# Kernel tuning notes

Measured on AMD Instinct MI355X. Metric: run time of the kernel, lower is better.

## Reference

```python
import jax, jax.numpy as jnp
import numpy as np

B, N, E, C1, C2 = 8, 4096, 2048, 128, 128
DENSITY = 0.05  # incidence matrix sparsity (stored dense, as in the original)


def setup_inputs() -> dict:
    key = jax.random.key(0)
    kx, kh, kw = jax.random.split(key, 3)
    x = jax.random.normal(kx, (B, N, C1), dtype=jnp.float32)
    # binary hypergraph incidence matrix [B, n_node, n_edge]
    H = (jax.random.uniform(kh, (B, N, E)) < DENSITY).astype(jnp.float32)
    W = jax.random.normal(kw, (C1, C2), dtype=jnp.float32) * 0.02
    b = jnp.zeros((C2,), dtype=jnp.float32)
    return {"x": x, "H": H, "W": W, "b": b}


def _mean_agg(path, X):
    # path: [B, T, S], X: [B, S, D] -> mean-aggregated [B, T, D]
    out = jnp.matmul(path, X)
    s = jnp.sum(path, axis=2, keepdims=True)  # [B, T, 1]
    # 1/s with inf (s==0) masked to 0, fused as a single where
    return jnp.where(s > 0, out / s, jnp.zeros_like(out))


def reference(x, H, W, b):
    # fc: [B, N, C1] -> [B, N, C2]
    x = jnp.matmul(x, W) + b
    # v2e: aggregate node features into hyperedge features
    Ht = jnp.swapaxes(H, 1, 2)  # [B, E, N]
    e = _mean_agg(Ht, x)        # [B, E, C2]
    # e2v: aggregate hyperedge features back to nodes
    v = _mean_agg(H, e)         # [B, N, C2]
    return v
```

## Files before the change

### kernel.cpp

```cpp
#include <hip/hip_runtime.h>
#include <stdint.h>

constexpr int B_ = 8, N_ = 4096, E_ = 2048, C_ = 128;
constexpr int KT  = 32;
constexpr int MT  = 64;
constexpr int NJW = 4;
constexpr int LRP = 65;

typedef short bf16x8 __attribute__((ext_vector_type(8)));
typedef float f32x4  __attribute__((ext_vector_type(4)));
typedef unsigned int u32x4 __attribute__((ext_vector_type(4)));

__device__ inline uint16_t bf16_rne(float f) {
    uint32_t u = __builtin_bit_cast(uint32_t, f);
    return (uint16_t)((u + 0x7FFFu + ((u >> 16) & 1u)) >> 16);
}

constexpr size_t BIT_B = (size_t)(N_ / 32) * E_;
constexpr size_t HT_E  = (size_t)B_ * BIT_B;
constexpr size_t WT_E  = (size_t)C_ * C_;
constexpr size_t EBF_E = (size_t)B_ * C_ * E_;
constexpr size_t RS_E  = (size_t)B_ * E_;
constexpr size_t RD_E  = (size_t)B_ * N_;

__global__ void pack_kernel(const float* __restrict__ H, uint32_t* __restrict__ HT,
                            uint32_t* __restrict__ HTe) {
    const int t  = threadIdx.x;
    const int eg = blockIdx.x & 7;
    const int ng = (blockIdx.x >> 3) & 127;
    const int b  = blockIdx.x >> 10;
    const int e  = eg * 256 + t;
    const float* hp = H + ((size_t)b * N_ + ng * 32) * E_ + e;
    uint32_t w = 0;
#pragma unroll
    for (int i = 0; i < 32; ++i) w |= (hp[(size_t)i * E_] > 0.5f) ? (1u << i) : 0u;
    HT[((size_t)b * (N_ / 32) + ng) * E_ + e] = w;

    const int lane  = t & 63;
    const int ebase = eg * 256 + (t >> 6) * 64;
    uint32_t val = 0;
#pragma unroll
    for (int i = 0; i < 32; ++i) {
        unsigned long long m = __ballot((w >> i) & 1u);
        uint32_t half = (lane < 32) ? (uint32_t)m : (uint32_t)(m >> 32);
        if ((lane & 31) == i) val = half;
    }
    HTe[((size_t)b * (E_ / 32) + (ebase >> 5) + (lane >> 5)) * N_ + ng * 32 + (lane & 31)] = val;
}

__global__ void prep_kernel(const float* __restrict__ W, const uint32_t* __restrict__ HT,
                            const uint32_t* __restrict__ HTe, uint16_t* __restrict__ WTb,
                            float* __restrict__ rs_e, float* __restrict__ rd_n) {
    const int blk = blockIdx.x, t = threadIdx.x;
    if (blk < 128) {
        const int i = blk * 256 + t;
        const int b = i >> 12, n = i & 4095;
        const uint32_t* p = HTe + (size_t)b * BIT_B + n;
        int s = 0;
#pragma unroll 1
        for (int ew = 0; ew < E_ / 32; ++ew) s += __popc(p[(size_t)ew * N_]);
        rd_n[i] = (s > 0) ? 0.5f / (float)s : 0.f;
    } else if (blk < 192) {
        const int i = (blk - 128) * 256 + t;
        const int b = i >> 11, e = i & 2047;
        const uint32_t* p = HT + (size_t)b * BIT_B + e;
        int s = 0;
#pragma unroll 1
        for (int ng = 0; ng < N_ / 32; ++ng) s += __popc(p[(size_t)ng * E_]);
        rs_e[i] = (s > 0) ? 0.5f / (float)s : 0.f;
    } else if (blk < 256) {
        const int i = (blk - 192) * 256 + t;
        const int c = i >> 7, k = i & 127;
        WTb[i] = bf16_rne(W[k * C_ + c]);
    }
}


#define LOADA(S, k0_) do {                                                            \
    if constexpr (MODE == 0) {                                                        \
        _Pragma("unroll")                                                             \
        for (int g = 0; g < NG; ++g) {                                                \
            const float* ap = Ax + ((size_t)batch * N_ + m0 + g * 16 + l15) * C_ + (k0_) + quad * 8; \
            const float4 f0 = *(const float4*)ap;                                     \
            const float4 f1 = *(const float4*)(ap + 4);                               \
            af##S[g*8+0]=f0.x; af##S[g*8+1]=f0.y; af##S[g*8+2]=f0.z; af##S[g*8+3]=f0.w; \
            af##S[g*8+4]=f1.x; af##S[g*8+5]=f1.y; af##S[g*8+6]=f1.z; af##S[g*8+7]=f1.w; \
        }                                                                             \
    } else {                                                                          \
        const uint32_t* p = Hp + (size_t)((k0_) >> 5) * RL + m0 + l15;                \
        _Pragma("unroll")                                                             \
        for (int g = 0; g < NG; ++g) aw##S[g] = p[g * 16];                            \
    } } while (0)

#define LOADB(S, k0_) do {                                                            \
    _Pragma("unroll")                                                                 \
    for (int j2 = 0; j2 < NJW; ++j2)                                                  \
        bq##S[j2] = *(const bf16x8*)&Bp[(size_t)((jw + j2) * 16 + l15) * K + (k0_) + quad * 8]; \
    } while (0)

#define MKFRAGS(S, A)                                                                 \
    bf16x8 A[NG];                                                                     \
    do {                                                                              \
    if constexpr (MODE == 0) {                                                        \
        _Pragma("unroll")                                                             \
        for (int g = 0; g < NG; ++g)                                                  \
            { _Pragma("unroll")                                                       \
              for (int jj = 0; jj < 8; ++jj) A[g][jj] = (short)bf16_rne(af##S[g*8+jj]); } \
    } else {                                                                          \
        const int qs = quad * 8;                                                      \
        _Pragma("unroll")                                                             \
        for (int g = 0; g < NG; ++g) {                                                \
            const uint32_t wv = aw##S[g];                                             \
            const uint32_t nb0 = (wv >> qs) & 0xFu;                                   \
            const uint32_t nb1 = (wv >> (qs + 4)) & 0xFu;                             \
            const uint32_t s0m = ((nb0 * 0x204081u) & 0x01010101u) << 6;              \
            const uint32_t s1m = ((nb1 * 0x204081u) & 0x01010101u) << 6;              \
            u32x4 qq = { __builtin_amdgcn_perm(s0m, 0u, 0x05000400u),                 \
                         __builtin_amdgcn_perm(s0m, 0u, 0x07000600u),                 \
                         __builtin_amdgcn_perm(s1m, 0u, 0x05000400u),                 \
                         __builtin_amdgcn_perm(s1m, 0u, 0x07000600u) };               \
            A[g] = __builtin_bit_cast(bf16x8, qq);                                    \
        }                                                                             \
    } } while (0)

template <int MODE>
__device__ __attribute__((always_inline))
void gemm_body(const float* __restrict__ Ax, const uint32_t* __restrict__ bits,
               const uint16_t* __restrict__ Btb, const float* __restrict__ bias,
               const float* __restrict__ rcp, uint16_t* __restrict__ outT,
               float* __restrict__ outF) {
    constexpr int K   = (MODE == 0) ? C_ : (MODE == 1) ? N_ : E_;
    constexpr int KH  = K / 2;
    constexpr int SW  = KH / KT;
    constexpr int OLD = (MODE == 0) ? N_ : E_;
    constexpr int RL  = (MODE == 1) ? E_ : N_;
    constexpr int NG  = MT / 16;
    static_assert(SW == 2 || (SW >= 4 && SW % 4 == 0), "pipeline shape");

    __shared__ float R[2 * 64 * LRP];

    const int t = threadIdx.x, wave = t >> 6, lane = t & 63;
    const int l15 = lane & 15, quad = lane >> 4;
    const int kh = wave & 1, jg = wave >> 1;
    const int jw = jg * NJW;
    const int kwv = kh * KH;
    const int batch = blockIdx.x & 7;
    const int m0 = (blockIdx.x >> 3) * MT;

    const uint16_t* Bp = Btb + (MODE == 0 ? (size_t)0 : (size_t)batch * C_ * K);
    const uint32_t* Hp = bits + (size_t)batch * BIT_B;

    f32x4 acc[NG * NJW];
    float    af0[NG * 8], af1[NG * 8], af2[NG * 8], af3[NG * 8];
    uint32_t aw0[NG], aw1[NG], aw2[NG], aw3[NG];
    bf16x8   bq0[NJW], bq1[NJW], bq2[NJW], bq3[NJW];

    auto mfma_all = [&](const bf16x8 (&A)[NG], const bf16x8 (&bv)[NJW])
        __attribute__((always_inline)) {
#pragma unroll
        for (int j2 = 0; j2 < NJW; ++j2)
#pragma unroll
            for (int g = 0; g < NG; ++g)
                acc[g * NJW + j2] = __builtin_amdgcn_mfma_f32_16x16x32_bf16(A[g], bv[j2], acc[g * NJW + j2], 0, 0, 0);
    };

#pragma unroll
    for (int i = 0; i < NG * NJW; ++i) acc[i] = (f32x4){0.f, 0.f, 0.f, 0.f};

    if constexpr (SW >= 4) {
        LOADA(0, kwv);          LOADB(0, kwv);
        LOADA(1, kwv + KT);     LOADB(1, kwv + KT);
        LOADA(2, kwv + 2 * KT); LOADB(2, kwv + 2 * KT);
        LOADA(3, kwv + 3 * KT); LOADB(3, kwv + 3 * KT);
#pragma unroll 1
        for (int s = 0; s < SW - 4; s += 4) {
            { MKFRAGS(0, A0); mfma_all(A0, bq0); LOADA(0, kwv + (s + 4) * KT); LOADB(0, kwv + (s + 4) * KT); }
            { MKFRAGS(1, A1); mfma_all(A1, bq1); LOADA(1, kwv + (s + 5) * KT); LOADB(1, kwv + (s + 5) * KT); }
            { MKFRAGS(2, A2); mfma_all(A2, bq2); LOADA(2, kwv + (s + 6) * KT); LOADB(2, kwv + (s + 6) * KT); }
            { MKFRAGS(3, A3); mfma_all(A3, bq3); LOADA(3, kwv + (s + 7) * KT); LOADB(3, kwv + (s + 7) * KT); }
        }
        { MKFRAGS(0, A0); mfma_all(A0, bq0); }
        { MKFRAGS(1, A1); mfma_all(A1, bq1); }
        { MKFRAGS(2, A2); mfma_all(A2, bq2); }
        { MKFRAGS(3, A3); mfma_all(A3, bq3); }
    } else {
        LOADA(0, kwv);      LOADB(0, kwv);
        LOADA(1, kwv + KT); LOADB(1, kwv + KT);
        { MKFRAGS(0, A0); mfma_all(A0, bq0); }
        { MKFRAGS(1, A1); mfma_all(A1, bq1); }
    }

    const int rbase = jg * 64 * LRP;
    if (kh == 1) {
#pragma unroll
        for (int g = 0; g < NG; ++g)
#pragma unroll
            for (int j2 = 0; j2 < NJW; ++j2)
#pragma unroll
                for (int r = 0; r < 4; ++r)
                    R[rbase + (g * 16 + quad * 4 + r) * LRP + j2 * 16 + l15] = acc[g * NJW + j2][r];
    }
    __syncthreads();
    if (kh != 0) return;
#pragma unroll
    for (int g = 0; g < NG; ++g)
#pragma unroll
        for (int j2 = 0; j2 < NJW; ++j2)
#pragma unroll
            for (int r = 0; r < 4; ++r)
                acc[g * NJW + j2][r] += R[rbase + (g * 16 + quad * 4 + r) * LRP + j2 * 16 + l15];

    float mul[NG][4];
    if constexpr (MODE != 0) {
#pragma unroll
        for (int g = 0; g < NG; ++g) {
            const float4 rv = *(const float4*)&rcp[(size_t)batch * RL + m0 + g * 16 + quad * 4];
            mul[g][0] = rv.x; mul[g][1] = rv.y; mul[g][2] = rv.z; mul[g][3] = rv.w;
        }
    }
#pragma unroll
    for (int g = 0; g < NG; ++g) {
        const int row = m0 + g * 16 + quad * 4;
        if constexpr (MODE == 2) {
            float* op = outF + ((size_t)batch * N_ + row) * C_;
#pragma unroll
            for (int j2 = 0; j2 < NJW; ++j2) {
                const int c = (jw + j2) * 16 + l15;
#pragma unroll
                for (int r = 0; r < 4; ++r) op[(size_t)r * C_ + c] = acc[g * NJW + j2][r] * mul[g][r];
            }
        } else {
#pragma unroll
            for (int j2 = 0; j2 < NJW; ++j2) {
                const int c = (jw + j2) * 16 + l15;
                float v0, v1, v2, v3;
                if constexpr (MODE == 0) {
                    float bb = bias[c];
                    v0 = acc[g * NJW + j2][0] + bb; v1 = acc[g * NJW + j2][1] + bb;
                    v2 = acc[g * NJW + j2][2] + bb; v3 = acc[g * NJW + j2][3] + bb;
                } else {
                    v0 = acc[g * NJW + j2][0] * mul[g][0]; v1 = acc[g * NJW + j2][1] * mul[g][1];
                    v2 = acc[g * NJW + j2][2] * mul[g][2]; v3 = acc[g * NJW + j2][3] * mul[g][3];
                }
                uint32_t q0 = (uint32_t)bf16_rne(v0) | ((uint32_t)bf16_rne(v1) << 16);
                uint32_t q1 = (uint32_t)bf16_rne(v2) | ((uint32_t)bf16_rne(v3) << 16);
                uint16_t* op = outT + ((size_t)batch * C_ + c) * OLD + row;
                *(uint2*)op = make_uint2(q0, q1);
            }
        }
    }
}

__global__ __launch_bounds__(256, 2)
void fc_k(const float* __restrict__ Ax, const uint16_t* __restrict__ Btb,
          const float* __restrict__ bias, uint16_t* __restrict__ outT) {
    gemm_body<0>(Ax, nullptr, Btb, bias, nullptr, outT, nullptr);
}
__global__ __launch_bounds__(256, 2)
void v2e_k(const uint32_t* __restrict__ HT, const uint16_t* __restrict__ Btb,
           const float* __restrict__ rcp, uint16_t* __restrict__ outT) {
    gemm_body<1>(nullptr, HT, Btb, nullptr, rcp, outT, nullptr);
}
__global__ __launch_bounds__(256, 2)
void e2v_k(const uint32_t* __restrict__ HTe, const uint16_t* __restrict__ Btb,
           const float* __restrict__ rcp, float* __restrict__ outF) {
    gemm_body<2>(nullptr, HTe, Btb, nullptr, rcp, nullptr, outF);
}

extern "C" void kernel_launch(void* const* d_in, const int* in_sizes, int n_in,
                              void* d_out, int out_size, void* d_ws, size_t ws_size,
                              hipStream_t stream) {
    const float* x    = (const float*)d_in[0];
    const float* H    = (const float*)d_in[1];
    const float* W    = (const float*)d_in[2];
    const float* bias = (const float*)d_in[3];
    float* out = (float*)d_out;

    uint32_t* HT   = (uint32_t*)d_ws;
    uint32_t* HTe  = HT + HT_E;
    uint16_t* WTb  = (uint16_t*)(HTe + HT_E);
    uint16_t* ebfT = WTb + WT_E;
    float*    rs_e = (float*)(ebfT + EBF_E);
    float*    rd_n = rs_e + RS_E;
    uint16_t* xwbT = (uint16_t*)d_out;

    pack_kernel<<<dim3(8192), dim3(256), 0, stream>>>(H, HT, HTe);
    prep_kernel<<<dim3(256), dim3(256), 0, stream>>>(W, HT, HTe, WTb, rs_e, rd_n);
    fc_k <<<dim3(8 * (N_ / MT)), dim3(256), 0, stream>>>(x, WTb, bias, xwbT);
    v2e_k<<<dim3(8 * (E_ / MT)), dim3(256), 0, stream>>>(HT, xwbT, rs_e, ebfT);
    e2v_k<<<dim3(8 * (N_ / MT)), dim3(256), 0, stream>>>(HTe, ebfT, rd_n, out);
}
```

Before: 465.7 us.

## Fuse H packing with fc GEMM and move bit transpose into prep kernel

The fc GEMM now runs as extra blocks inside the H-packing launch and converts W to bf16 on the fly, which removes the separate fc launch and the WTb buffer. Packing now reads float4 and writes uint4, so each thread handles four edges. The ballot-based bit transpose (HTe) and the per-node degree counts move into the prep kernel, which builds them from HT instead of rereading H. Fewer launches and wider loads on the dominant 268MB read of H are the intent. The cost is strided scalar W reads inside the fc blocks and a larger prep kernel that rereads HT.

New measurement: 477.5 us. 2.5% more time.

```diff
diff --git a/kernel.cpp b/kernel.cpp
--- a/kernel.cpp
+++ b/kernel.cpp
@@ -4,8 +4,8 @@
 constexpr int B_ = 8, N_ = 4096, E_ = 2048, C_ = 128;
 constexpr int KT  = 32;
 constexpr int MT  = 64;
-constexpr int NJW = 4;
 constexpr int LRP = 65;
+constexpr int PACK_BLKS = 2048;
 
 typedef short bf16x8 __attribute__((ext_vector_type(8)));
 typedef float f32x4  __attribute__((ext_vector_type(4)));
@@ -18,62 +18,9 @@
 
 constexpr size_t BIT_B = (size_t)(N_ / 32) * E_;
 constexpr size_t HT_E  = (size_t)B_ * BIT_B;
-constexpr size_t WT_E  = (size_t)C_ * C_;
 constexpr size_t EBF_E = (size_t)B_ * C_ * E_;
 constexpr size_t RS_E  = (size_t)B_ * E_;
 constexpr size_t RD_E  = (size_t)B_ * N_;
-
-__global__ void pack_kernel(const float* __restrict__ H, uint32_t* __restrict__ HT,
-                            uint32_t* __restrict__ HTe) {
-    const int t  = threadIdx.x;
-    const int eg = blockIdx.x & 7;
-    const int ng = (blockIdx.x >> 3) & 127;
-    const int b  = blockIdx.x >> 10;
-    const int e  = eg * 256 + t;
-    const float* hp = H + ((size_t)b * N_ + ng * 32) * E_ + e;
-    uint32_t w = 0;
-#pragma unroll
-    for (int i = 0; i < 32; ++i) w |= (hp[(size_t)i * E_] > 0.5f) ? (1u << i) : 0u;
-    HT[((size_t)b * (N_ / 32) + ng) * E_ + e] = w;
-
-    const int lane  = t & 63;
-    const int ebase = eg * 256 + (t >> 6) * 64;
-    uint32_t val = 0;
-#pragma unroll
-    for (int i = 0; i < 32; ++i) {
-        unsigned long long m = __ballot((w >> i) & 1u);
-        uint32_t half = (lane < 32) ? (uint32_t)m : (uint32_t)(m >> 32);
-        if ((lane & 31) == i) val = half;
-    }
-    HTe[((size_t)b * (E_ / 32) + (ebase >> 5) + (lane >> 5)) * N_ + ng * 32 + (lane & 31)] = val;
-}
-
-__global__ void prep_kernel(const float* __restrict__ W, const uint32_t* __restrict__ HT,
-                            const uint32_t* __restrict__ HTe, uint16_t* __restrict__ WTb,
-                            float* __restrict__ rs_e, float* __restrict__ rd_n) {
-    const int blk = blockIdx.x, t = threadIdx.x;
-    if (blk < 128) {
-        const int i = blk * 256 + t;
-        const int b = i >> 12, n = i & 4095;
-        const uint32_t* p = HTe + (size_t)b * BIT_B + n;
-        int s = 0;
-#pragma unroll 1
-        for (int ew = 0; ew < E_ / 32; ++ew) s += __popc(p[(size_t)ew * N_]);
-        rd_n[i] = (s > 0) ? 0.5f / (float)s : 0.f;
-    } else if (blk < 192) {
-        const int i = (blk - 128) * 256 + t;
-        const int b = i >> 11, e = i & 2047;
-        const uint32_t* p = HT + (size_t)b * BIT_B + e;
-        int s = 0;
-#pragma unroll 1
-        for (int ng = 0; ng < N_ / 32; ++ng) s += __popc(p[(size_t)ng * E_]);
-        rs_e[i] = (s > 0) ? 0.5f / (float)s : 0.f;
-    } else if (blk < 256) {
-        const int i = (blk - 192) * 256 + t;
-        const int c = i >> 7, k = i & 127;
-        WTb[i] = bf16_rne(W[k * C_ + c]);
-    }
-}
 
 
 #define LOADA(S, k0_) do {                                                            \
@@ -93,10 +40,19 @@
     } } while (0)
 
 #define LOADB(S, k0_) do {                                                            \
-    _Pragma("unroll")                                                                 \
-    for (int j2 = 0; j2 < NJW; ++j2)                                                  \
-        bq##S[j2] = *(const bf16x8*)&Bp[(size_t)((jw + j2) * 16 + l15) * K + (k0_) + quad * 8]; \
-    } while (0)
+    if constexpr (MODE == 0) {                                                        \
+        _Pragma("unroll")                                                             \
+        for (int j2 = 0; j2 < NJWm; ++j2) {                                           \
+            const int c = (jw + j2) * 16 + l15;                                       \
+            _Pragma("unroll")                                                         \
+            for (int jj = 0; jj < 8; ++jj)                                            \
+                bq##S[j2][jj] = (short)bf16_rne(Wf[(size_t)((k0_) + quad * 8 + jj) * C_ + c]); \
+        }                                                                             \
+    } else {                                                                          \
+        _Pragma("unroll")                                                             \
+        for (int j2 = 0; j2 < NJWm; ++j2)                                             \
+            bq##S[j2] = *(const bf16x8*)&Bp[(size_t)((jw + j2) * 16 + l15) * K + (k0_) + quad * 8]; \
+    } } while (0)
 
 #define MKFRAGS(S, A)                                                                 \
     bf16x8 A[NG];                                                                     \
@@ -125,49 +81,57 @@
 
 template <int MODE>
 __device__ __attribute__((always_inline))
-void gemm_body(const float* __restrict__ Ax, const uint32_t* __restrict__ bits,
-               const uint16_t* __restrict__ Btb, const float* __restrict__ bias,
-               const float* __restrict__ rcp, uint16_t* __restrict__ outT,
-               float* __restrict__ outF) {
-    constexpr int K   = (MODE == 0) ? C_ : (MODE == 1) ? N_ : E_;
-    constexpr int KH  = K / 2;
-    constexpr int SW  = KH / KT;
-    constexpr int OLD = (MODE == 0) ? N_ : E_;
-    constexpr int RL  = (MODE == 1) ? E_ : N_;
-    constexpr int NG  = MT / 16;
-    static_assert(SW == 2 || (SW >= 4 && SW % 4 == 0), "pipeline shape");
-
-    __shared__ float R[2 * 64 * LRP];
+void gemm_body(int bid, const float* __restrict__ Ax, const uint32_t* __restrict__ bits,
+               const uint16_t* __restrict__ Btb, const float* __restrict__ Wf,
+               const float* __restrict__ bias, const float* __restrict__ rcp,
+               uint16_t* __restrict__ outT, float* __restrict__ outF) {
+    constexpr int K    = (MODE == 0) ? C_ : (MODE == 1) ? N_ : E_;
+    constexpr int NJWm = (MODE == 0) ? 2 : 4;
+    constexpr int KH   = (MODE == 0) ? K : K / 2;
+    constexpr int SW   = KH / KT;
+    constexpr int OLD  = (MODE == 0) ? N_ : E_;
+    constexpr int RL   = (MODE == 1) ? E_ : N_;
+    constexpr int NG   = MT / 16;
+
+    __shared__ float R[(MODE == 0) ? 1 : (2 * 64 * LRP)];
 
     const int t = threadIdx.x, wave = t >> 6, lane = t & 63;
     const int l15 = lane & 15, quad = lane >> 4;
-    const int kh = wave & 1, jg = wave >> 1;
-    const int jw = jg * NJW;
+    const int kh = (MODE == 0) ? 0 : (wave & 1);
+    const int jg = (MODE == 0) ? wave : (wave >> 1);
+    const int jw = jg * NJWm;
     const int kwv = kh * KH;
-    const int batch = blockIdx.x & 7;
-    const int m0 = (blockIdx.x >> 3) * MT;
+    const int batch = bid & 7;
+    const int m0 = (bid >> 3) * MT;
 
     const uint16_t* Bp = Btb + (MODE == 0 ? (size_t)0 : (size_t)batch * C_ * K);
     const uint32_t* Hp = bits + (size_t)batch * BIT_B;
 
-    f32x4 acc[NG * NJW];
+    f32x4 acc[NG * NJWm];
     float    af0[NG * 8], af1[NG * 8], af2[NG * 8], af3[NG * 8];
     uint32_t aw0[NG], aw1[NG], aw2[NG], aw3[NG];
-    bf16x8   bq0[NJW], bq1[NJW], bq2[NJW], bq3[NJW];
-
-    auto mfma_all = [&](const bf16x8 (&A)[NG], const bf16x8 (&bv)[NJW])
+    bf16x8   bq0[NJWm], bq1[NJWm], bq2[NJWm], bq3[NJWm];
+
+    auto mfma_all = [&](const bf16x8 (&A)[NG], const bf16x8 (&bv)[NJWm])
         __attribute__((always_inline)) {
 #pragma unroll
-        for (int j2 = 0; j2 < NJW; ++j2)
+        for (int j2 = 0; j2 < NJWm; ++j2)
 #pragma unroll
             for (int g = 0; g < NG; ++g)
-                acc[g * NJW + j2] = __builtin_amdgcn_mfma_f32_16x16x32_bf16(A[g], bv[j2], acc[g * NJW + j2], 0, 0, 0);
+                acc[g * NJWm + j2] = __builtin_amdgcn_mfma_f32_16x16x32_bf16(A[g], bv[j2], acc[g * NJWm + j2], 0, 0, 0);
     };
 
 #pragma unroll
-    for (int i = 0; i < NG * NJW; ++i) acc[i] = (f32x4){0.f, 0.f, 0.f, 0.f};
-
-    if constexpr (SW >= 4) {
+    for (int i = 0; i < NG * NJWm; ++i) acc[i] = (f32x4){0.f, 0.f, 0.f, 0.f};
+
+    if constexpr (MODE == 0) {
+        LOADA(0, 0);  LOADB(0, 0);
+        LOADA(1, KT); LOADB(1, KT);
+        { MKFRAGS(0, A0); mfma_all(A0, bq0); LOADA(0, 2 * KT); LOADB(0, 2 * KT); }
+        { MKFRAGS(1, A1); mfma_all(A1, bq1); LOADA(1, 3 * KT); LOADB(1, 3 * KT); }
+        { MKFRAGS(0, A0); mfma_all(A0, bq0); }
+        { MKFRAGS(1, A1); mfma_all(A1, bq1); }
+    } else {
         LOADA(0, kwv);          LOADB(0, kwv);
         LOADA(1, kwv + KT);     LOADB(1, kwv + KT);
         LOADA(2, kwv + 2 * KT); LOADB(2, kwv + 2 * KT);
@@ -183,32 +147,27 @@
         { MKFRAGS(1, A1); mfma_all(A1, bq1); }
         { MKFRAGS(2, A2); mfma_all(A2, bq2); }
         { MKFRAGS(3, A3); mfma_all(A3, bq3); }
-    } else {
-        LOADA(0, kwv);      LOADB(0, kwv);
-        LOADA(1, kwv + KT); LOADB(1, kwv + KT);
-        { MKFRAGS(0, A0); mfma_all(A0, bq0); }
-        { MKFRAGS(1, A1); mfma_all(A1, bq1); }
-    }
-
-    const int rbase = jg * 64 * LRP;
-    if (kh == 1) {
+
+        const int rbase = jg * 64 * LRP;
+        if (kh == 1) {
+#pragma unroll
+            for (int g = 0; g < NG; ++g)
+#pragma unroll
+                for (int j2 = 0; j2 < NJWm; ++j2)
+#pragma unroll
+                    for (int r = 0; r < 4; ++r)
+                        R[rbase + (g * 16 + quad * 4 + r) * LRP + j2 * 16 + l15] = acc[g * NJWm + j2][r];
+        }
+        __syncthreads();
+        if (kh != 0) return;
 #pragma unroll
         for (int g = 0; g < NG; ++g)
 #pragma unroll
-            for (int j2 = 0; j2 < NJW; ++j2)
+            for (int j2 = 0; j2 < NJWm; ++j2)
 #pragma unroll
                 for (int r = 0; r < 4; ++r)
-                    R[rbase + (g * 16 + quad * 4 + r) * LRP + j2 * 16 + l15] = acc[g * NJW + j2][r];
-    }
-    __syncthreads();
-    if (kh != 0) return;
-#pragma unroll
-    for (int g = 0; g < NG; ++g)
-#pragma unroll
-        for (int j2 = 0; j2 < NJW; ++j2)
-#pragma unroll
-            for (int r = 0; r < 4; ++r)
-                acc[g * NJW + j2][r] += R[rbase + (g * 16 + quad * 4 + r) * LRP + j2 * 16 + l15];
+                    acc[g * NJWm + j2][r] += R[rbase + (g * 16 + quad * 4 + r) * LRP + j2 * 16 + l15];
+    }
 
     float mul[NG][4];
     if constexpr (MODE != 0) {
@@ -224,23 +183,23 @@
         if constexpr (MODE == 2) {
             float* op = outF + ((size_t)batch * N_ + row) * C_;
 #pragma unroll
-            for (int j2 = 0; j2 < NJW; ++j2) {
+            for (int j2 = 0; j2 < NJWm; ++j2) {
                 const int c = (jw + j2) * 16 + l15;
 #pragma unroll
-                for (int r = 0; r < 4; ++r) op[(size_t)r * C_ + c] = acc[g * NJW + j2][r] * mul[g][r];
+                for (int r = 0; r < 4; ++r) op[(size_t)r * C_ + c] = acc[g * NJWm + j2][r] * mul[g][r];
             }
         } else {
 #pragma unroll
-            for (int j2 = 0; j2 < NJW; ++j2) {
+            for (int j2 = 0; j2 < NJWm; ++j2) {
                 const int c = (jw + j2) * 16 + l15;
                 float v0, v1, v2, v3;
                 if constexpr (MODE == 0) {
                     float bb = bias[c];
-                    v0 = acc[g * NJW + j2][0] + bb; v1 = acc[g * NJW + j2][1] + bb;
-                    v2 = acc[g * NJW + j2][2] + bb; v3 = acc[g * NJW + j2][3] + bb;
+                    v0 = acc[g * NJWm + j2][0] + bb; v1 = acc[g * NJWm + j2][1] + bb;
+                    v2 = acc[g * NJWm + j2][2] + bb; v3 = acc[g * NJWm + j2][3] + bb;
                 } else {
-                    v0 = acc[g * NJW + j2][0] * mul[g][0]; v1 = acc[g * NJW + j2][1] * mul[g][1];
-                    v2 = acc[g * NJW + j2][2] * mul[g][2]; v3 = acc[g * NJW + j2][3] * mul[g][3];
+                    v0 = acc[g * NJWm + j2][0] * mul[g][0]; v1 = acc[g * NJWm + j2][1] * mul[g][1];
+                    v2 = acc[g * NJWm + j2][2] * mul[g][2]; v3 = acc[g * NJWm + j2][3] * mul[g][3];
                 }
                 uint32_t q0 = (uint32_t)bf16_rne(v0) | ((uint32_t)bf16_rne(v1) << 16);
                 uint32_t q1 = (uint32_t)bf16_rne(v2) | ((uint32_t)bf16_rne(v3) << 16);
@@ -252,19 +211,84 @@
 }
 
 __global__ __launch_bounds__(256, 2)
-void fc_k(const float* __restrict__ Ax, const uint16_t* __restrict__ Btb,
-          const float* __restrict__ bias, uint16_t* __restrict__ outT) {
-    gemm_body<0>(Ax, nullptr, Btb, bias, nullptr, outT, nullptr);
-}
+void pack_fc_k(const float* __restrict__ H, uint32_t* __restrict__ HT,
+               const float* __restrict__ x, const float* __restrict__ W,
+               const float* __restrict__ bias, uint16_t* __restrict__ xwbT) {
+    if (blockIdx.x >= PACK_BLKS) {
+        gemm_body<0>(blockIdx.x - PACK_BLKS, x, nullptr, nullptr, W, bias, nullptr, xwbT, nullptr);
+        return;
+    }
+    const int t  = threadIdx.x;
+    const int eg = blockIdx.x & 1;
+    const int ng = (blockIdx.x >> 1) & 127;
+    const int b  = blockIdx.x >> 8;
+    const int e0 = eg * 1024 + t * 4;
+    const float* hp = H + ((size_t)b * N_ + ng * 32) * E_ + e0;
+    uint32_t w0 = 0, w1 = 0, w2 = 0, w3 = 0;
+#pragma unroll
+    for (int i = 0; i < 32; ++i) {
+        const float4 f = *(const float4*)(hp + (size_t)i * E_);
+        w0 |= (f.x > 0.5f) ? (1u << i) : 0u;
+        w1 |= (f.y > 0.5f) ? (1u << i) : 0u;
+        w2 |= (f.z > 0.5f) ? (1u << i) : 0u;
+        w3 |= (f.w > 0.5f) ? (1u << i) : 0u;
+    }
+    *(uint4*)&HT[((size_t)b * (N_ / 32) + ng) * E_ + e0] = make_uint4(w0, w1, w2, w3);
+}
+
+__global__ void prep_kernel(const uint32_t* __restrict__ HT, uint32_t* __restrict__ HTe,
+                            float* __restrict__ rs_e, float* __restrict__ rd_n) {
+    const int blk = blockIdx.x, t = threadIdx.x;
+    const int wave = t >> 6, lane = t & 63;
+    if (blk < 256) {
+        const int wid = blk * 4 + wave;
+        const int b = wid >> 7, ng = wid & 127;
+        const uint32_t* p = HT + ((size_t)b * (N_ / 32) + ng) * E_;
+        int cnt = 0;
+#pragma unroll 1
+        for (int c8 = 0; c8 < E_ / 64; ++c8) {
+            const uint32_t w = p[c8 * 64 + lane];
+#pragma unroll
+            for (int i = 0; i < 32; ++i) {
+                unsigned long long m = __ballot((w >> i) & 1u);
+                if (lane == i) cnt += __popcll(m);
+            }
+        }
+        if (lane < 32)
+            rd_n[(size_t)b * N_ + ng * 32 + lane] = (cnt > 0) ? 0.5f / (float)cnt : 0.f;
+    } else if (blk < 320) {
+        const int i = (blk - 256) * 256 + t;
+        const int b = i >> 11, e = i & 2047;
+        const uint32_t* p = HT + (size_t)b * BIT_B + e;
+        int s = 0;
+#pragma unroll 1
+        for (int ng = 0; ng < N_ / 32; ++ng) s += __popc(p[(size_t)ng * E_]);
+        rs_e[i] = (s > 0) ? 0.5f / (float)s : 0.f;
+    } else {
+        const int wid = (blk - 320) * 4 + wave;
+        const int b = wid >> 12, rest = wid & 4095;
+        const int ng = rest >> 5, eg64 = rest & 31;
+        const uint32_t w = HT[((size_t)b * (N_ / 32) + ng) * E_ + eg64 * 64 + lane];
+        uint32_t val = 0;
+#pragma unroll
+        for (int i = 0; i < 32; ++i) {
+            unsigned long long m = __ballot((w >> i) & 1u);
+            uint32_t half = (lane < 32) ? (uint32_t)m : (uint32_t)(m >> 32);
+            if ((lane & 31) == i) val = half;
+        }
+        HTe[((size_t)b * (E_ / 32) + eg64 * 2 + (lane >> 5)) * N_ + ng * 32 + (lane & 31)] = val;
+    }
+}
+
 __global__ __launch_bounds__(256, 2)
 void v2e_k(const uint32_t* __restrict__ HT, const uint16_t* __restrict__ Btb,
            const float* __restrict__ rcp, uint16_t* __restrict__ outT) {
-    gemm_body<1>(nullptr, HT, Btb, nullptr, rcp, outT, nullptr);
+    gemm_body<1>(blockIdx.x, nullptr, HT, Btb, nullptr, nullptr, rcp, outT, nullptr);
 }
 __global__ __launch_bounds__(256, 2)
 void e2v_k(const uint32_t* __restrict__ HTe, const uint16_t* __restrict__ Btb,
            const float* __restrict__ rcp, float* __restrict__ outF) {
-    gemm_body<2>(nullptr, HTe, Btb, nullptr, rcp, nullptr, outF);
+    gemm_body<2>(blockIdx.x, nullptr, HTe, Btb, nullptr, nullptr, rcp, nullptr, outF);
 }
 
 extern "C" void kernel_launch(void* const* d_in, const int* in_sizes, int n_in,
@@ -278,15 +302,13 @@
 
     uint32_t* HT   = (uint32_t*)d_ws;
     uint32_t* HTe  = HT + HT_E;
-    uint16_t* WTb  = (uint16_t*)(HTe + HT_E);
-    uint16_t* ebfT = WTb + WT_E;
+    uint16_t* ebfT = (uint16_t*)(HTe + HT_E);
     float*    rs_e = (float*)(ebfT + EBF_E);
     float*    rd_n = rs_e + RS_E;
     uint16_t* xwbT = (uint16_t*)d_out;
 
-    pack_kernel<<<dim3(8192), dim3(256), 0, stream>>>(H, HT, HTe);
-    prep_kernel<<<dim3(256), dim3(256), 0, stream>>>(W, HT, HTe, WTb, rs_e, rd_n);
-    fc_k <<<dim3(8 * (N_ / MT)), dim3(256), 0, stream>>>(x, WTb, bias, xwbT);
+    pack_fc_k<<<dim3(PACK_BLKS + 8 * (N_ / MT)), dim3(256), 0, stream>>>(H, HT, x, W, bias, xwbT);
+    prep_kernel<<<dim3(8512), dim3(256), 0, stream>>>(HT, HTe, rs_e, rd_n);
     v2e_k<<<dim3(8 * (E_ / MT)), dim3(256), 0, stream>>>(HT, xwbT, rs_e, ebfT);
     e2v_k<<<dim3(8 * (N_ / MT)), dim3(256), 0, stream>>>(HTe, ebfT, rd_n, out);
 }
```
